# Performance work log

Hardware: AMD Instinct MI355X
Metric: run time of the kernel (lower is better)

The kernel has to match this reference:

```python
import jax, jax.numpy as jnp
import numpy as np


def setup_inputs() -> dict:
    key = jax.random.key(0)
    ks = jax.random.split(key, 7)
    B, T, X, H, Y = 256, 2048, 64, 128, 32
    s_ih = 1.0 / np.sqrt(H)
    return {
        "x": jax.random.normal(ks[0], (B, T, X), dtype=jnp.float32),
        "W_ih": jax.random.normal(ks[1], (H, X), dtype=jnp.float32) * s_ih,
        "W_hh": jax.random.normal(ks[2], (H, H), dtype=jnp.float32) * s_ih,
        "b_ih": jax.random.normal(ks[3], (H,), dtype=jnp.float32) * s_ih,
        "b_hh": jax.random.normal(ks[4], (H,), dtype=jnp.float32) * s_ih,
        "W_out": jax.random.normal(ks[5], (Y, H), dtype=jnp.float32) * s_ih,
        "b_out": jax.random.normal(ks[6], (Y,), dtype=jnp.float32) * s_ih,
    }


def reference(x, W_ih, W_hh, b_ih, b_hh, W_out, b_out):
    # Vanilla tanh RNN (torch.nn.RNN, 1 layer, batch_first), zero initial state,
    # readout on the last timestep: h_t = tanh(x_t W_ih^T + b_ih + h_{t-1} W_hh^T + b_hh)
    B, T, X = x.shape
    H = W_hh.shape[0]
    # Precompute input projections for all timesteps in one big GEMM: [T, B, H]
    xs = (jnp.einsum('bti,hi->bth', x, W_ih) + (b_ih + b_hh)).transpose(1, 0, 2)

    def step(h, xt):
        h = jnp.tanh(xt + h @ W_hh.T)
        return h, None

    h0 = jnp.zeros((B, H), dtype=x.dtype)
    h_last, _ = jax.lax.scan(step, h0, xs)
    out = h_last @ W_out.T + b_out  # [B, Y]
    return out
```

## Files before the change

kernel.cpp:

```cpp
#include <hip/hip_runtime.h>

#define TT 2048
#define BB 256
#define XX 64
#define HH 128
#define YY 32
#define SSTR 12
#define HBUF (16 * SSTR)


typedef float v2f __attribute__((ext_vector_type(2)));
typedef float v4f __attribute__((ext_vector_type(4)));

#define PKFMA(acc, a, b)                                              \
    asm("v_pk_fma_f32 %0, %1, %2, %0 op_sel:[0,0,0] op_sel_hi:[1,1,1]"\
        : "+v"(acc) : "v"(a), "v"(b))

template<int CTRL>
static __device__ __forceinline__ float dpp_mov(float s) {
    return __int_as_float(__builtin_amdgcn_update_dpp(
        0, __float_as_int(s), CTRL, 0xF, 0xF, true));
}

static __device__ __forceinline__ void pin2(v2f& v) {
    asm volatile("" : "+v"(v));
}

#define LO2(v) __builtin_shufflevector(v, v, 0, 1)
#define HI2(v) __builtin_shufflevector(v, v, 2, 3)

__global__ __launch_bounds__(1024)
__attribute__((amdgpu_waves_per_eu(4, 4)))
void rnn_persist_kernel(const float* __restrict__ x,
                        const float* __restrict__ W_ih,
                        const float* __restrict__ W_hh,
                        const float* __restrict__ b_ih,
                        const float* __restrict__ b_hh,
                        const float* __restrict__ W_out,
                        const float* __restrict__ b_out,
                        float* __restrict__ out)
{
    __shared__ __align__(16) float h_lds[2][HBUF];

    const int tid  = threadIdx.x;
    const int b    = blockIdx.x;
    const int w    = tid >> 6;
    const int lane = tid & 63;
    const int kg   = lane & 15;
    const int jgl  = lane >> 4;
    const int jg   = w * 4 + jgl;
    const int j0   = jg * 2;
    const int b3   = (lane >> 3) & 1;

    const float SC = 2.8853900817779268f;

    v2f whh2[2][4];
    v2f wih2[2][2];
    float bs[2];
    #pragma unroll
    for (int jj = 0; jj < 2; ++jj) {
        const v2f* ph = (const v2f*)(W_hh + (j0 + jj) * HH + kg * 8);
        #pragma unroll
        for (int c = 0; c < 4; ++c) whh2[jj][c] = ph[c] * SC;
        const v2f* pi = (const v2f*)(W_ih + (j0 + jj) * XX + kg * 4);
        #pragma unroll
        for (int c = 0; c < 2; ++c) wih2[jj][c] = pi[c] * SC;
        bs[jj] = (b_ih[j0 + jj] + b_hh[j0 + jj]) * SC;
    }
    #pragma unroll
    for (int jj = 0; jj < 2; ++jj) {
        #pragma unroll
        for (int c = 0; c < 4; ++c) pin2(whh2[jj][c]);
        pin2(wih2[jj][0]); pin2(wih2[jj][1]);
    }
    const float bsel = b3 ? bs[1] : bs[0];
    const int   jw   = j0 + b3;
    const int   woff = (jw >> 3) * SSTR + (jw & 7);
    const bool  writer = (lane & 7) == 0;

    const float* xg = x + (size_t)b * TT * XX + kg * 4;

    if (tid < HBUF) h_lds[0][tid] = 0.f;

    v2f sxA0 = {0.f, 0.f}, sxA1 = {0.f, 0.f};
    v2f sxB0, sxB1;
    {
        const v4f x0 = *(const v4f*)xg;
        PKFMA(sxA0, wih2[0][0], LO2(x0)); PKFMA(sxA0, wih2[0][1], HI2(x0));
        PKFMA(sxA1, wih2[1][0], LO2(x0)); PKFMA(sxA1, wih2[1][1], HI2(x0));
    }
    v4f xa = *(const v4f*)(xg + XX);
    v4f xb = *(const v4f*)(xg + 2 * XX);
    __syncthreads();

#define STEP(RP, WP, SXU0, SXU1, SXF0, SXF1, XSRC, PRE, XPF)               \
    do {                                                                   \
        const v4f* hp = (const v4f*)&h_lds[RP][kg * SSTR];                 \
        const v4f H0 = hp[0], H1 = hp[1];                                  \
        v2f a0 = SXU0, a1 = SXU1;                                          \
        PKFMA(a0, whh2[0][0], LO2(H0)); PKFMA(a0, whh2[0][1], HI2(H0));    \
        PKFMA(a0, whh2[0][2], LO2(H1)); PKFMA(a0, whh2[0][3], HI2(H1));    \
        PKFMA(a1, whh2[1][0], LO2(H0)); PKFMA(a1, whh2[1][1], HI2(H0));    \
        PKFMA(a1, whh2[1][2], LO2(H1)); PKFMA(a1, whh2[1][3], HI2(H1));    \
        float s0 = a0.x + a0.y;                                            \
        float s1 = a1.x + a1.y;                                            \
        s0 += dpp_mov<0xB1>(s0);  s1 += dpp_mov<0xB1>(s1);       \
        s0 += dpp_mov<0x4E>(s0);  s1 += dpp_mov<0x4E>(s1);       \
        float u  = b3 ? s1 : s0;                                           \
        float vv = b3 ? s0 : s1;                                           \
        u += dpp_mov<0x128>(vv);      \
        u += dpp_mov<0x141>(u);          \
        u += bsel;                          \
        const float e  = __builtin_amdgcn_exp2f(u);                        \
        const float hn = fmaf(-2.f, __builtin_amdgcn_rcpf(e + 1.f), 1.f); \
        if (writer) h_lds[WP][woff] = hn;                                  \
                   \
        SXF0 = (v2f){0.f, 0.f}; SXF1 = (v2f){0.f, 0.f};                    \
        PKFMA(SXF0, wih2[0][0], LO2(XSRC)); PKFMA(SXF0, wih2[0][1], HI2(XSRC)); \
        PKFMA(SXF1, wih2[1][0], LO2(XSRC)); PKFMA(SXF1, wih2[1][1], HI2(XSRC)); \
        { const int tn_ = (PRE) < TT ? (PRE) : TT - 1;                     \
          XPF = *(const v4f*)(xg + (size_t)tn_ * XX); }                    \
        __syncthreads();                                                   \
    } while (0)

    for (int t = 0; t < TT; t += 2) {
        STEP(0, 1, sxA0, sxA1, sxB0, sxB1, xa, t + 3, xa);
        STEP(1, 0, sxB0, sxB1, sxA0, sxA1, xb, t + 4, xb);
    }
#undef STEP

    if (tid < YY) {
        const float* h  = h_lds[0];
        const float* wr = W_out + tid * HH;
        float r0 = 0.f, r1 = 0.f, r2 = 0.f, r3 = 0.f;
        #pragma unroll
        for (int s16 = 0; s16 < 16; ++s16) {
            #pragma unroll
            for (int c = 0; c < 2; ++c) {
                const float4 wv = *(const float4*)(wr + s16 * 8 + c * 4);
                const float4 hv = *(const float4*)(h + s16 * SSTR + c * 4);
                r0 = fmaf(wv.x, hv.x, r0); r1 = fmaf(wv.y, hv.y, r1);
                r2 = fmaf(wv.z, hv.z, r2); r3 = fmaf(wv.w, hv.w, r3);
            }
        }
        out[b * YY + tid] = b_out[tid] + ((r0 + r1) + (r2 + r3));
    }
}

extern "C" void kernel_launch(void* const* d_in, const int* in_sizes, int n_in,
                              void* d_out, int out_size, void* d_ws, size_t ws_size,
                              hipStream_t stream) {
    const float* x     = (const float*)d_in[0];
    const float* W_ih  = (const float*)d_in[1];
    const float* W_hh  = (const float*)d_in[2];
    const float* b_ih  = (const float*)d_in[3];
    const float* b_hh  = (const float*)d_in[4];
    const float* W_out = (const float*)d_in[5];
    const float* b_out = (const float*)d_in[6];
    float* out = (float*)d_out;

    rnn_persist_kernel<<<BB, 1024, 0, stream>>>(x, W_ih, W_hh, b_ih, b_hh,
                                                W_out, b_out, out);
}
```

Before: 722.9 us.

## Halve block size, compute four hidden units per lane group, custom LDS barrier

```diff
diff --git a/kernel.cpp b/kernel.cpp
--- a/kernel.cpp
+++ b/kernel.cpp
@@ -26,11 +26,17 @@
     asm volatile("" : "+v"(v));
 }
 
+static __device__ __forceinline__ void barrier_lgkm() {
+    asm volatile("s_waitcnt lgkmcnt(0)" ::: "memory");
+    __builtin_amdgcn_s_barrier();
+    asm volatile("" ::: "memory");
+}
+
 #define LO2(v) __builtin_shufflevector(v, v, 0, 1)
 #define HI2(v) __builtin_shufflevector(v, v, 2, 3)
 
-__global__ __launch_bounds__(1024)
-__attribute__((amdgpu_waves_per_eu(4, 4)))
+__global__ __launch_bounds__(512)
+__attribute__((amdgpu_waves_per_eu(2, 2)))
 void rnn_persist_kernel(const float* __restrict__ x,
                         const float* __restrict__ W_ih,
                         const float* __restrict__ W_hh,
@@ -47,85 +53,91 @@
     const int w    = tid >> 6;
     const int lane = tid & 63;
     const int kg   = lane & 15;
-    const int jgl  = lane >> 4;
-    const int jg   = w * 4 + jgl;
-    const int j0   = jg * 2;
-    const int b3   = (lane >> 3) & 1;
+    const int jp   = lane >> 4;
+    const int j0   = (w * 4 + jp) * 4;
+    const int b0   = lane & 1;
+    const int b1   = (lane >> 1) & 1;
+    const int o    = lane & 3;
+    const int jw   = j0 + o;
+    const int woff = (jw >> 3) * SSTR + (jw & 7);
+    const bool writer = (lane & 12) == 0;
 
     const float SC = 2.8853900817779268f;
 
-    v2f whh2[2][4];
-    v2f wih2[2][2];
-    float bs[2];
+    v2f whh2[4][4];
+    v2f wih2[4][2];
     #pragma unroll
-    for (int jj = 0; jj < 2; ++jj) {
+    for (int jj = 0; jj < 4; ++jj) {
         const v2f* ph = (const v2f*)(W_hh + (j0 + jj) * HH + kg * 8);
         #pragma unroll
         for (int c = 0; c < 4; ++c) whh2[jj][c] = ph[c] * SC;
         const v2f* pi = (const v2f*)(W_ih + (j0 + jj) * XX + kg * 4);
         #pragma unroll
         for (int c = 0; c < 2; ++c) wih2[jj][c] = pi[c] * SC;
-        bs[jj] = (b_ih[j0 + jj] + b_hh[j0 + jj]) * SC;
     }
     #pragma unroll
-    for (int jj = 0; jj < 2; ++jj) {
+    for (int jj = 0; jj < 4; ++jj) {
         #pragma unroll
         for (int c = 0; c < 4; ++c) pin2(whh2[jj][c]);
         pin2(wih2[jj][0]); pin2(wih2[jj][1]);
     }
-    const float bsel = b3 ? bs[1] : bs[0];
-    const int   jw   = j0 + b3;
-    const int   woff = (jw >> 3) * SSTR + (jw & 7);
-    const bool  writer = (lane & 7) == 0;
+    const float bsel = (b_ih[jw] + b_hh[jw]) * SC;
 
     const float* xg = x + (size_t)b * TT * XX + kg * 4;
 
     if (tid < HBUF) h_lds[0][tid] = 0.f;
 
-    v2f sxA0 = {0.f, 0.f}, sxA1 = {0.f, 0.f};
-    v2f sxB0, sxB1;
-    {
-        const v4f x0 = *(const v4f*)xg;
-        PKFMA(sxA0, wih2[0][0], LO2(x0)); PKFMA(sxA0, wih2[0][1], HI2(x0));
-        PKFMA(sxA1, wih2[1][0], LO2(x0)); PKFMA(sxA1, wih2[1][1], HI2(x0));
-    }
-    v4f xa = *(const v4f*)(xg + XX);
-    v4f xb = *(const v4f*)(xg + 2 * XX);
+    v4f xa = *(const v4f*)xg;
+    v4f xb = *(const v4f*)(xg + XX);
     __syncthreads();
 
-#define STEP(RP, WP, SXU0, SXU1, SXF0, SXF1, XSRC, PRE, XPF)               \
+#define STEP(RP, WP, XC)                                                   \
     do {                                                                   \
         const v4f* hp = (const v4f*)&h_lds[RP][kg * SSTR];                 \
         const v4f H0 = hp[0], H1 = hp[1];                                  \
-        v2f a0 = SXU0, a1 = SXU1;                                          \
-        PKFMA(a0, whh2[0][0], LO2(H0)); PKFMA(a0, whh2[0][1], HI2(H0));    \
-        PKFMA(a0, whh2[0][2], LO2(H1)); PKFMA(a0, whh2[0][3], HI2(H1));    \
-        PKFMA(a1, whh2[1][0], LO2(H0)); PKFMA(a1, whh2[1][1], HI2(H0));    \
-        PKFMA(a1, whh2[1][2], LO2(H1)); PKFMA(a1, whh2[1][3], HI2(H1));    \
-        float s0 = a0.x + a0.y;                                            \
-        float s1 = a1.x + a1.y;                                            \
-        s0 += dpp_mov<0xB1>(s0);  s1 += dpp_mov<0xB1>(s1);       \
-        s0 += dpp_mov<0x4E>(s0);  s1 += dpp_mov<0x4E>(s1);       \
-        float u  = b3 ? s1 : s0;                                           \
-        float vv = b3 ? s0 : s1;                                           \
-        u += dpp_mov<0x128>(vv);      \
-        u += dpp_mov<0x141>(u);          \
+        const v2f h2[4] = { LO2(H0), HI2(H0), LO2(H1), HI2(H1) };          \
+        const v2f x2[2] = { LO2(XC), HI2(XC) };                            \
+        float s[4];                                                        \
+        _Pragma("unroll")                                                  \
+        for (int jj = 0; jj < 4; ++jj) {                                   \
+            v2f a = {0.f, 0.f};                                            \
+            PKFMA(a, wih2[jj][0], x2[0]); PKFMA(a, wih2[jj][1], x2[1]);    \
+            PKFMA(a, whh2[jj][0], h2[0]); PKFMA(a, whh2[jj][1], h2[1]);    \
+            PKFMA(a, whh2[jj][2], h2[2]); PKFMA(a, whh2[jj][3], h2[3]);    \
+            s[jj] = a.x + a.y;                                             \
+        }                                                                  \
+                           \
+        float ul = b0 ? s[1] : s[0];                                       \
+        float vl = b0 ? s[0] : s[1];                                       \
+        ul += dpp_mov<0xB1>(vl);                                           \
+        float uh = b0 ? s[3] : s[2];                                       \
+        float vh = b0 ? s[2] : s[3];                                       \
+        uh += dpp_mov<0xB1>(vh);                                           \
+                           \
+        float u  = b1 ? uh : ul;                                           \
+        float vv = b1 ? ul : uh;                                           \
+        u += dpp_mov<0x4E>(vv);                                            \
+        \
+        u += dpp_mov<0x124>(u);                             \
+        u += dpp_mov<0x128>(u);                             \
         u += bsel;                          \
         const float e  = __builtin_amdgcn_exp2f(u);                        \
         const float hn = fmaf(-2.f, __builtin_amdgcn_rcpf(e + 1.f), 1.f); \
         if (writer) h_lds[WP][woff] = hn;                                  \
-                   \
-        SXF0 = (v2f){0.f, 0.f}; SXF1 = (v2f){0.f, 0.f};                    \
-        PKFMA(SXF0, wih2[0][0], LO2(XSRC)); PKFMA(SXF0, wih2[0][1], HI2(XSRC)); \
-        PKFMA(SXF1, wih2[1][0], LO2(XSRC)); PKFMA(SXF1, wih2[1][1], HI2(XSRC)); \
-        { const int tn_ = (PRE) < TT ? (PRE) : TT - 1;                     \
-          XPF = *(const v4f*)(xg + (size_t)tn_ * XX); }                    \
-        __syncthreads();                                                   \
+        barrier_lgkm();                                                    \
     } while (0)
 
     for (int t = 0; t < TT; t += 2) {
-        STEP(0, 1, sxA0, sxA1, sxB0, sxB1, xa, t + 3, xa);
-        STEP(1, 0, sxB0, sxB1, sxA0, sxA1, xb, t + 4, xb);
+        STEP(0, 1, xa);
+        {
+            const int tn = (t + 2 < TT) ? t + 2 : TT - 1;
+            xa = *(const v4f*)(xg + (size_t)tn * XX);
+        }
+        STEP(1, 0, xb);
+        {
+            const int tn = (t + 3 < TT) ? t + 3 : TT - 1;
+            xb = *(const v4f*)(xg + (size_t)tn * XX);
+        }
     }
 #undef STEP
 
@@ -159,6 +171,6 @@
     const float* b_out = (const float*)d_in[6];
     float* out = (float*)d_out;
 
-    rnn_persist_kernel<<<BB, 1024, 0, stream>>>(x, W_ih, W_hh, b_ih, b_hh,
-                                                W_out, b_out, out);
+    rnn_persist_kernel<<<BB, 512, 0, stream>>>(x, W_ih, W_hh, b_ih, b_hh,
+                                               W_out, b_out, out);
 }
```

Result: faster. 619.1 us (-14.4%).
